# Performance work log

Hardware: AMD Instinct MI355X
Metric: run time of the kernel (lower is better)

Reference implementation:

```python
import jax, jax.numpy as jnp
import numpy as np

D = 128
EMB = 1024
B, S = 4, 4096


def setup_inputs() -> dict:
    key = jax.random.key(0)
    ks = jax.random.split(key, 7)
    scale = 1.0 / np.sqrt(EMB)
    return {
        "X": jax.random.normal(ks[0], (B, S, EMB), dtype=jnp.float32),
        "lam": jnp.float32(0.8),
        "Wq": jax.random.uniform(ks[1], (EMB, 2 * D), jnp.float32, -scale, scale),
        "bq": jax.random.uniform(ks[2], (2 * D,), jnp.float32, -scale, scale),
        "Wk": jax.random.uniform(ks[3], (EMB, 2 * D), jnp.float32, -scale, scale),
        "bk": jax.random.uniform(ks[4], (2 * D,), jnp.float32, -scale, scale),
        "Wv": jax.random.uniform(ks[5], (EMB, D), jnp.float32, -scale, scale),
        "bv": jax.random.uniform(ks[6], (D,), jnp.float32, -scale, scale),
    }


def reference(X, lam, Wq, bq, Wk, bk, Wv, bv):
    # Projections: Q,K are [B,S,2d]; V is [B,S,d]
    Q = X @ Wq + bq
    K = X @ Wk + bk
    V = X @ Wv + bv
    Q1, Q2 = Q[..., :D], Q[..., D:]
    K1, K2 = K[..., :D], K[..., D:]
    s = 1.0 / jnp.sqrt(jnp.float32(D))
    # Dual QK^T scores [B,S,S]
    A1 = jnp.einsum("bqd,bkd->bqk", Q1, K1) * s
    A2 = jnp.einsum("bqd,bkd->bqk", Q2, K2) * s
    P = jax.nn.softmax(A1, axis=-1) - lam * jax.nn.softmax(A2, axis=-1)
    return jnp.einsum("bqk,bkd->bqd", P, V)
```

## Files before the change

### kernel.cpp

```cpp
#include <hip/hip_runtime.h>
#include <hip/hip_bf16.h>


typedef __attribute__((ext_vector_type(8))) short bf16x8;
typedef __attribute__((ext_vector_type(4))) float f32x4;
typedef __attribute__((ext_vector_type(16))) float f32x16;

#define MFMA16(a, b, c) __builtin_amdgcn_mfma_f32_16x16x32_bf16((a), (b), (c), 0, 0, 0)
#define MFMA32(a, b, c) __builtin_amdgcn_mfma_f32_32x32x16_bf16((a), (b), (c), 0, 0, 0)

typedef const __attribute__((address_space(1))) void gas_void;
typedef __attribute__((address_space(3))) void las_void;
#define GLOAD16(G, L) __builtin_amdgcn_global_load_lds((gas_void*)(G), (las_void*)(L), 16, 0, 0)

__device__ __forceinline__ unsigned short f2bf(float x) {
    union { float f; unsigned u; } v; v.f = x;
    return (unsigned short)((v.u + 0x7FFFu + ((v.u >> 16) & 1u)) >> 16);
}
__device__ __forceinline__ unsigned pk2bf(float a, float b) {
    __hip_bfloat162 h = __float22bfloat162_rn(float2{a, b});
    union { __hip_bfloat162 h2; unsigned u; } cv; cv.h2 = h;
    return cv.u;
}
__device__ __forceinline__ float fexp2(float x) {
    float r; asm("v_exp_f32 %0, %1" : "=v"(r) : "v"(x)); return r;
}

__global__ __launch_bounds__(256) void wtrans_kernel(
    const float* __restrict__ Wq, const float* __restrict__ Wk,
    const float* __restrict__ Wv, unsigned short* __restrict__ Wt) {
    int tid = blockIdx.x * 256 + threadIdx.x;
    int k = tid & 1023, n = tid >> 10;
    float v;
    if (n < 256)      v = Wq[k * 256 + n];
    else if (n < 512) v = Wk[k * 256 + (n - 256)];
    else              v = Wv[k * 128 + (n - 512)];
    Wt[tid] = f2bf(v);
}

__global__ __launch_bounds__(256) void proj_kernel(
    const float* __restrict__ X, const unsigned short* __restrict__ Wt,
    const float* __restrict__ bq, const float* __restrict__ bk,
    const float* __restrict__ bv,
    unsigned short* __restrict__ Qs, unsigned short* __restrict__ Kb,
    unsigned short* __restrict__ Vb) {
    __shared__ alignas(16) char lds[16384];
    const int nt = blockIdx.y;
    const int m0 = blockIdx.x * 128;
    const int t = threadIdx.x, w = t >> 6, l = t & 63, c = l & 15, g = l >> 4;
    const int wm = w >> 1, wn = w & 1;
    const unsigned short* Wrow = Wt + (long)(nt * 128) * 1024;

    f32x4 acc[4][4];
    const f32x4 fz = {0.f, 0.f, 0.f, 0.f};
#pragma unroll
    for (int i = 0; i < 4; i++)
#pragma unroll
        for (int j = 0; j < 4; j++) acc[i][j] = fz;

    const int srow = t >> 1, sh = t & 1;
    const int sswz = (srow & 7) << 4;
    for (int k0 = 0; k0 < 1024; k0 += 32) {
        const float* xs = X + (long)(m0 + srow) * 1024 + k0 + sh * 16;
        float4 f0 = *(const float4*)(xs + 0);
        float4 f1 = *(const float4*)(xs + 4);
        float4 f2 = *(const float4*)(xs + 8);
        float4 f3 = *(const float4*)(xs + 12);
        const unsigned short* wsc = Wrow + (long)srow * 1024 + k0 + sh * 16;
        uint4 w0 = *(const uint4*)(wsc + 0);
        uint4 w1 = *(const uint4*)(wsc + 8);
        uint4 xa, xb;
        xa.x = pk2bf(f0.x, f0.y); xa.y = pk2bf(f0.z, f0.w);
        xa.z = pk2bf(f1.x, f1.y); xa.w = pk2bf(f1.z, f1.w);
        xb.x = pk2bf(f2.x, f2.y); xb.y = pk2bf(f2.z, f2.w);
        xb.z = pk2bf(f3.x, f3.y); xb.w = pk2bf(f3.z, f3.w);
        int base = srow * 64 + sh * 32;
        *(uint4*)(lds + ((base + 0) ^ sswz)) = xa;
        *(uint4*)(lds + ((base + 16) ^ sswz)) = xb;
        *(uint4*)(lds + 8192 + ((base + 0) ^ sswz)) = w0;
        *(uint4*)(lds + 8192 + ((base + 16) ^ sswz)) = w1;
        __syncthreads();

        bf16x8 af[4];
#pragma unroll
        for (int am = 0; am < 4; am++) {
            int r_ = wm * 64 + am * 16 + c;
            af[am] = *(const bf16x8*)(lds + ((r_ * 64 + g * 16) ^ ((c & 7) << 4)));
        }
#pragma unroll
        for (int bn = 0; bn < 4; bn++) {
            int r_ = wn * 64 + bn * 16 + c;
            bf16x8 bfr = *(const bf16x8*)(lds + 8192 + ((r_ * 64 + g * 16) ^ ((c & 7) << 4)));
#pragma unroll
            for (int am = 0; am < 4; am++) acc[am][bn] = MFMA16(af[am], bfr, acc[am][bn]);
        }
        __syncthreads();
    }

    const float QSCALE = 0.08838834764831845f * 1.4426950408889634f;
    const float* bias; float scale; unsigned short* outp; int ostride, ocol0, boff;
    if (nt < 2)      { bias = bq; boff = nt * 128;       scale = QSCALE; outp = Qs; ostride = 256; ocol0 = nt * 128; }
    else if (nt < 4) { bias = bk; boff = (nt - 2) * 128; scale = 1.0f;   outp = Kb; ostride = 256; ocol0 = (nt - 2) * 128; }
    else             { bias = bv; boff = 0;              scale = 1.0f;   outp = Vb; ostride = 128; ocol0 = 0; }
#pragma unroll
    for (int bn = 0; bn < 4; bn++) {
        int ncol = wn * 64 + bn * 16 + c;
        float bb = bias[boff + ncol];
#pragma unroll
        for (int am = 0; am < 4; am++) {
#pragma unroll
            for (int r = 0; r < 4; r++) {
                long row = m0 + wm * 64 + am * 16 + 4 * g + r;
                outp[row * ostride + ocol0 + ncol] = f2bf((acc[am][bn][r] + bb) * scale);
            }
        }
    }
}

__global__ __launch_bounds__(256) void vtrans_kernel(
    const unsigned short* __restrict__ Vb, unsigned short* __restrict__ Vt) {
    int tid = blockIdx.x * 256 + threadIdx.x;
    int s = tid & 4095, d = (tid >> 12) & 127, b = tid >> 19;
    Vt[tid] = Vb[(((long)b << 12) + s) * 128 + d];
}

__global__ __launch_bounds__(512) void attn3_kernel(
    const unsigned short* __restrict__ Qs, const unsigned short* __restrict__ Kb,
    const unsigned short* __restrict__ Vt,
    float* __restrict__ Po, float* __restrict__ Ps, int nsplit, int ks) {
    __shared__ alignas(16) char lds[98304];
    const int t = threadIdx.x;
    const int w = t >> 6, l = t & 63, r31 = l & 31, hi = l >> 5;
    const int wq = w >> 1, br = w & 1;

    const int total = gridDim.x;
    const int lin = (blockIdx.x & 7) * (total >> 3) + (blockIdx.x >> 3);
    const int grp = lin >> 5, qb = lin & 31;
    const int b = grp / nsplit, split = grp % nsplit;

    const long qrow = (long)b * 4096 + qb * 128 + wq * 32 + r31;
    bf16x8 qf[8];
    const unsigned short* Qp = Qs + qrow * 256 + br * 128 + hi * 8;
#pragma unroll
    for (int ds = 0; ds < 8; ds++) qf[ds] = *(const bf16x8*)(Qp + ds * 16);

    f32x16 o[4];
    const f32x16 oz = {};
#pragma unroll
    for (int dt = 0; dt < 4; dt++) o[dt] = oz;
    float m = -1e30f, s = 0.f;

    const int krow = w * 4 + (l >> 4);
    const int kc = (l & 15) * 16;
    const int ksrc_rot = (kc - krow * 16) & 255;
    const int vd = w * 16 + (l >> 2);
    const int vc = (l & 3) * 16;
    const long kbb = (long)b * 4096;
    const char* KbB = (const char*)Kb;
    const char* VtB = (const char*)Vt + ((long)b * 128 + vd) * 8192 +
                      ((vc - ((vd >> 1) & 3) * 16) & 63);
    char* dst0 = lds + w * 1024;

    const int kb0 = split * ks, kend = kb0 + ks;
#define STAGE(KB_, BUF_)                                                       \
    {                                                                          \
        const char* s1_ = KbB + (kbb + (KB_) + krow) * 512 + ksrc_rot;         \
        char* d_ = dst0 + (BUF_)*24576;                                        \
        GLOAD16(s1_, d_);                                                      \
        GLOAD16(s1_ + 256, d_ + 8192);                                         \
        GLOAD16(VtB + (long)(KB_)*2, d_ + 16384);                              \
    }

    int kro[8];
#pragma unroll
    for (int ds = 0; ds < 8; ds++)
        kro[ds] = br * 8192 + r31 * 256 + ((ds * 32 + hi * 16 + r31 * 16) & 255);
    int vro0[4], vro1[4];
#pragma unroll
    for (int dt = 0; dt < 4; dt++) {
        int vr = dt * 32 + r31, rot = ((vr >> 1) & 3) * 16;
        vro0[dt] = 16384 + vr * 64 + ((hi * 16 + rot) & 63);
        vro1[dt] = 16384 + vr * 64 + ((32 + hi * 16 + rot) & 63);
    }

    STAGE(kb0, 0);
    STAGE(kb0 + 32, 1);
    STAGE(kb0 + 64, 2);
    int cur = 0;

    for (int kb = kb0; kb < kend; kb += 32) {
        asm volatile("s_waitcnt vmcnt(6)" ::: "memory");
        __builtin_amdgcn_sched_barrier(0);
        __builtin_amdgcn_s_barrier();
        asm volatile("" ::: "memory");
        __builtin_amdgcn_sched_barrier(0);

        {
            int kn = kb + 96;
            if (kn >= kend) kn = kb0;
            STAGE(kn, (cur + 3) & 3);
        }
        const char* bufp = lds + cur * 24576;

        f32x16 pa = oz, pb_ = oz;
        __builtin_amdgcn_s_setprio(1);
#pragma unroll
        for (int ds = 0; ds < 4; ds++) {
            bf16x8 kfa = *(const bf16x8*)(bufp + kro[ds]);
            bf16x8 kfb = *(const bf16x8*)(bufp + kro[ds + 4]);
            pa = MFMA32(kfa, qf[ds], pa);
            pb_ = MFMA32(kfb, qf[ds + 4], pb_);
        }
        __builtin_amdgcn_s_setprio(0);
        f32x16 p;
#pragma unroll
        for (int i = 0; i < 16; i++) p[i] = pa[i] + pb_[i];

        float x0 = fmaxf(fmaxf(p[0], p[1]), fmaxf(p[2], p[3]));
        float x1 = fmaxf(fmaxf(p[4], p[5]), fmaxf(p[6], p[7]));
        float x2 = fmaxf(fmaxf(p[8], p[9]), fmaxf(p[10], p[11]));
        float x3 = fmaxf(fmaxf(p[12], p[13]), fmaxf(p[14], p[15]));
        float lmx = fmaxf(fmaxf(x0, x1), fmaxf(x2, x3));
        lmx = fmaxf(lmx, __shfl_xor(lmx, 32));
        if (__any(lmx > m + 8.f)) {
            float mn = fmaxf(m, lmx);
            float al = fexp2(m - mn);
            s *= al; m = mn;
#pragma unroll
            for (int dt = 0; dt < 4; dt++) o[dt] *= al;
        }
        float pe[16];
#pragma unroll
        for (int i = 0; i < 16; i++) pe[i] = fexp2(p[i] - m);
        float s0 = (pe[0] + pe[1]) + (pe[2] + pe[3]);
        float s1 = (pe[4] + pe[5]) + (pe[6] + pe[7]);
        float s2 = (pe[8] + pe[9]) + (pe[10] + pe[11]);
        float s3 = (pe[12] + pe[13]) + (pe[14] + pe[15]);
        float ps_ = (s0 + s1) + (s2 + s3);
        ps_ += __shfl_xor(ps_, 32);
        s += ps_;

        unsigned cA = pk2bf(pe[0], pe[1]), cB = pk2bf(pe[2], pe[3]);
        unsigned cC = pk2bf(pe[4], pe[5]), cD = pk2bf(pe[6], pe[7]);
        asm volatile("v_permlane32_swap_b32 %0, %1" : "+v"(cA), "+v"(cC));
        asm volatile("v_permlane32_swap_b32 %0, %1" : "+v"(cB), "+v"(cD));
        unsigned dA = pk2bf(pe[8], pe[9]), dB = pk2bf(pe[10], pe[11]);
        unsigned dC = pk2bf(pe[12], pe[13]), dD = pk2bf(pe[14], pe[15]);
        asm volatile("v_permlane32_swap_b32 %0, %1" : "+v"(dA), "+v"(dC));
        asm volatile("v_permlane32_swap_b32 %0, %1" : "+v"(dB), "+v"(dD));
        union { uint4 u; bf16x8 v; } pb0, pb1;
        pb0.u = uint4{cA, cB, cC, cD};
        pb1.u = uint4{dA, dB, dC, dD};

        __builtin_amdgcn_s_setprio(1);
#pragma unroll
        for (int dt = 0; dt < 4; dt++) {
            bf16x8 vf0 = *(const bf16x8*)(bufp + vro0[dt]);
            bf16x8 vf1 = *(const bf16x8*)(bufp + vro1[dt]);
            o[dt] = MFMA32(vf0, pb0.v, o[dt]);
            o[dt] = MFMA32(vf1, pb1.v, o[dt]);
        }
        __builtin_amdgcn_s_setprio(0);
        cur = (cur + 1) & 3;
    }

    float* po = Po + ((qrow * nsplit + split) * 2 + br) * 128;
#pragma unroll
    for (int dt = 0; dt < 4; dt++) {
#pragma unroll
        for (int rg = 0; rg < 4; rg++) {
            float4 v;
            v.x = o[dt][rg * 4 + 0];
            v.y = o[dt][rg * 4 + 1];
            v.z = o[dt][rg * 4 + 2];
            v.w = o[dt][rg * 4 + 3];
            *(float4*)(po + dt * 32 + rg * 8 + hi * 4) = v;
        }
    }
    if (hi == 0)
        *(float2*)(Ps + (qrow * nsplit + split) * 4 + br * 2) = float2{m, s};
}

__global__ __launch_bounds__(256) void combine_kernel(
    const float* __restrict__ Po, const float* __restrict__ Ps,
    const float* __restrict__ lam_p, float* __restrict__ out, int nsplit) {
    int tid = blockIdx.x * 256 + threadIdx.x;
    int q = tid >> 5, dq = (tid & 31) * 4;
    float M1 = -1e30f, M2 = -1e30f;
    for (int s = 0; s < nsplit; s++) {
        float4 st = *(const float4*)(Ps + (long)(q * nsplit + s) * 4);
        M1 = fmaxf(M1, st.x); M2 = fmaxf(M2, st.z);
    }
    float S1 = 0.f, S2 = 0.f;
    float a0 = 0.f, a1 = 0.f, a2 = 0.f, a3 = 0.f;
    float b0 = 0.f, b1 = 0.f, b2 = 0.f, b3 = 0.f;
    for (int s = 0; s < nsplit; s++) {
        float4 st = *(const float4*)(Ps + (long)(q * nsplit + s) * 4);
        float w1 = fexp2(st.x - M1), w2 = fexp2(st.z - M2);
        S1 += st.y * w1; S2 += st.w * w2;
        const float* p1 = Po + (((long)q * nsplit + s) * 2 + 0) * 128 + dq;
        const float* p2 = Po + (((long)q * nsplit + s) * 2 + 1) * 128 + dq;
        float4 v1 = *(const float4*)p1;
        float4 v2 = *(const float4*)p2;
        a0 += v1.x * w1; a1 += v1.y * w1; a2 += v1.z * w1; a3 += v1.w * w1;
        b0 += v2.x * w2; b1 += v2.y * w2; b2 += v2.z * w2; b3 += v2.w * w2;
    }
    float lam = *lam_p;
    float i1 = 1.f / S1, i2 = lam / S2;
    float4 v;
    v.x = a0 * i1 - b0 * i2;
    v.y = a1 * i1 - b1 * i2;
    v.z = a2 * i1 - b2 * i2;
    v.w = a3 * i1 - b3 * i2;
    *(float4*)(out + (long)q * 128 + dq) = v;
}

extern "C" void kernel_launch(void* const* d_in, const int* in_sizes, int n_in,
                              void* d_out, int out_size, void* d_ws, size_t ws_size,
                              hipStream_t stream) {
    const float* X   = (const float*)d_in[0];
    const float* lam = (const float*)d_in[1];
    const float* Wq  = (const float*)d_in[2];
    const float* bq  = (const float*)d_in[3];
    const float* Wk  = (const float*)d_in[4];
    const float* bk  = (const float*)d_in[5];
    const float* Wv  = (const float*)d_in[6];
    const float* bv  = (const float*)d_in[7];
    char* ws = (char*)d_ws;
    unsigned short* Qs = (unsigned short*)(ws);
    unsigned short* Kb = (unsigned short*)(ws + (8u << 20));
    unsigned short* Vb = (unsigned short*)(ws + (16u << 20));
    unsigned short* Vt = (unsigned short*)(ws + (20u << 20));
    unsigned short* Wt = (unsigned short*)(ws + (24u << 20));
    const size_t base = (size_t)26 << 20;
    const size_t NQ = 16384;
    int nsplit = 1;
    if (ws_size >= base + NQ * 4 * 2 * 128 * 4 + NQ * 4 * 4 * 4)      nsplit = 4;
    else if (ws_size >= base + NQ * 2 * 2 * 128 * 4 + NQ * 2 * 4 * 4) nsplit = 2;
    float* Po = (float*)(ws + base);
    float* Ps = (float*)(ws + base + NQ * (size_t)nsplit * 2 * 128 * 4);

    wtrans_kernel<<<2560, 256, 0, stream>>>(Wq, Wk, Wv, Wt);
    proj_kernel<<<dim3(128, 5), 256, 0, stream>>>(X, Wt, bq, bk, bv, Qs, Kb, Vb);
    vtrans_kernel<<<8192, 256, 0, stream>>>(Vb, Vt);
    attn3_kernel<<<128 * nsplit, 512, 0, stream>>>(Qs, Kb, Vt, Po, Ps,
                                                   nsplit, 4096 / nsplit);
    combine_kernel<<<2048, 256, 0, stream>>>(Po, Ps, lam, (float*)d_out, nsplit);
}
```

Before: 174.9 us.

## Software-pipeline QK^T of next tile with softmax and PV of current tile

Restructures the attention main loop so the QK^T MFMAs for tile i+1 are issued alongside the softmax and PV MFMAs for tile i, using two ping-pong score registers and a loop unrolled by two. The aim is to overlap MFMA work with exp/reduction VALU work and hide LDS latency. Barrier waits change from vmcnt(6) to vmcnt(3), and the s_setprio hints are dropped. It raises register pressure with an extra f32x16 live score tile and assumes the tile count is even and at least 2.

```diff
diff --git a/kernel.cpp b/kernel.cpp
--- a/kernel.cpp
+++ b/kernel.cpp
@@ -162,6 +162,7 @@
     char* dst0 = lds + w * 1024;
 
     const int kb0 = split * ks, kend = kb0 + ks;
+    const int nt = ks >> 5;
 #define STAGE(KB_, BUF_)                                                       \
     {                                                                          \
         const char* s1_ = KbB + (kbb + (KB_) + krow) * 512 + ksrc_rot;         \
@@ -183,86 +184,98 @@
         vro1[dt] = 16384 + vr * 64 + ((32 + hi * 16 + rot) & 63);
     }
 
+#define FENCE_TOP(N)                                                           \
+    asm volatile("s_waitcnt vmcnt(" #N ")" ::: "memory");                      \
+    __builtin_amdgcn_sched_barrier(0);                                         \
+    __builtin_amdgcn_s_barrier();                                              \
+    __builtin_amdgcn_sched_barrier(0);
+
+#define QKTILE(PN, TI)                                                         \
+    {                                                                          \
+        const char* kp_ = lds + ((TI) & 3) * 24576;                            \
+        f32x16 qa_ = oz, qb_ = oz;                                             \
+        _Pragma("unroll") for (int d_ = 0; d_ < 4; d_++) {                     \
+            bf16x8 ka_ = *(const bf16x8*)(kp_ + kro[d_]);                      \
+            bf16x8 kb_ = *(const bf16x8*)(kp_ + kro[d_ + 4]);                  \
+            qa_ = MFMA32(ka_, qf[d_], qa_);                                    \
+            qb_ = MFMA32(kb_, qf[d_ + 4], qb_);                                \
+        }                                                                      \
+        _Pragma("unroll") for (int i_ = 0; i_ < 16; i_++)                      \
+            PN[i_] = qa_[i_] + qb_[i_];                                        \
+    }
+
+#define SOFTPV(PC, TI)                                                         \
+    {                                                                          \
+        float x0 = fmaxf(fmaxf(PC[0], PC[1]), fmaxf(PC[2], PC[3]));            \
+        float x1 = fmaxf(fmaxf(PC[4], PC[5]), fmaxf(PC[6], PC[7]));            \
+        float x2 = fmaxf(fmaxf(PC[8], PC[9]), fmaxf(PC[10], PC[11]));          \
+        float x3 = fmaxf(fmaxf(PC[12], PC[13]), fmaxf(PC[14], PC[15]));        \
+        float lmx = fmaxf(fmaxf(x0, x1), fmaxf(x2, x3));                       \
+        lmx = fmaxf(lmx, __shfl_xor(lmx, 32));                                 \
+        if (__any(lmx > m + 8.f)) {                                            \
+            float mn = fmaxf(m, lmx);                                          \
+            float al = fexp2(m - mn);                                          \
+            s *= al; m = mn;                                                   \
+            _Pragma("unroll") for (int dt_ = 0; dt_ < 4; dt_++) o[dt_] *= al;  \
+        }                                                                      \
+        float pe[16];                                                          \
+        _Pragma("unroll") for (int i_ = 0; i_ < 16; i_++)                      \
+            pe[i_] = fexp2(PC[i_] - m);                                        \
+        float s0 = (pe[0] + pe[1]) + (pe[2] + pe[3]);                          \
+        float s1 = (pe[4] + pe[5]) + (pe[6] + pe[7]);                          \
+        float s2 = (pe[8] + pe[9]) + (pe[10] + pe[11]);                        \
+        float s3 = (pe[12] + pe[13]) + (pe[14] + pe[15]);                      \
+        float ps_ = (s0 + s1) + (s2 + s3);                                     \
+        ps_ += __shfl_xor(ps_, 32);                                            \
+        s += ps_;                                                              \
+        unsigned cA = pk2bf(pe[0], pe[1]), cB = pk2bf(pe[2], pe[3]);           \
+        unsigned cC = pk2bf(pe[4], pe[5]), cD = pk2bf(pe[6], pe[7]);           \
+        asm volatile("v_permlane32_swap_b32 %0, %1" : "+v"(cA), "+v"(cC));     \
+        asm volatile("v_permlane32_swap_b32 %0, %1" : "+v"(cB), "+v"(cD));     \
+        unsigned dA = pk2bf(pe[8], pe[9]), dB = pk2bf(pe[10], pe[11]);         \
+        unsigned dC = pk2bf(pe[12], pe[13]), dD = pk2bf(pe[14], pe[15]);       \
+        asm volatile("v_permlane32_swap_b32 %0, %1" : "+v"(dA), "+v"(dC));     \
+        asm volatile("v_permlane32_swap_b32 %0, %1" : "+v"(dB), "+v"(dD));     \
+        union { uint4 u; bf16x8 v; } pb0_, pb1_;                               \
+        pb0_.u = uint4{cA, cB, cC, cD};                                        \
+        pb1_.u = uint4{dA, dB, dC, dD};                                        \
+        const char* vb_ = lds + ((TI) & 3) * 24576;                            \
+        _Pragma("unroll") for (int dt_ = 0; dt_ < 4; dt_++) {                  \
+            bf16x8 vf0 = *(const bf16x8*)(vb_ + vro0[dt_]);                    \
+            bf16x8 vf1 = *(const bf16x8*)(vb_ + vro1[dt_]);                    \
+            o[dt_] = MFMA32(vf0, pb0_.v, o[dt_]);                              \
+            o[dt_] = MFMA32(vf1, pb1_.v, o[dt_]);                              \
+        }                                                                      \
+    }
+
+#define STEP(PC, PN, I)                                                        \
+    {                                                                          \
+        FENCE_TOP(3)                                                           \
+        {                                                                      \
+            int i3_ = (I) + 3;                                                 \
+            int kn_ = (i3_ < nt) ? kb0 + (i3_ << 5) : kb0;                     \
+            STAGE(kn_, i3_ & 3);                                               \
+        }                                                                      \
+        QKTILE(PN, (I) + 1)                                                    \
+        SOFTPV(PC, (I))                                                        \
+    }
+
     STAGE(kb0, 0);
     STAGE(kb0 + 32, 1);
     STAGE(kb0 + 64, 2);
-    int cur = 0;
-
-    for (int kb = kb0; kb < kend; kb += 32) {
-        asm volatile("s_waitcnt vmcnt(6)" ::: "memory");
-        __builtin_amdgcn_sched_barrier(0);
-        __builtin_amdgcn_s_barrier();
-        asm volatile("" ::: "memory");
-        __builtin_amdgcn_sched_barrier(0);
-
-        {
-            int kn = kb + 96;
-            if (kn >= kend) kn = kb0;
-            STAGE(kn, (cur + 3) & 3);
-        }
-        const char* bufp = lds + cur * 24576;
-
-        f32x16 pa = oz, pb_ = oz;
-        __builtin_amdgcn_s_setprio(1);
-#pragma unroll
-        for (int ds = 0; ds < 4; ds++) {
-            bf16x8 kfa = *(const bf16x8*)(bufp + kro[ds]);
-            bf16x8 kfb = *(const bf16x8*)(bufp + kro[ds + 4]);
-            pa = MFMA32(kfa, qf[ds], pa);
-            pb_ = MFMA32(kfb, qf[ds + 4], pb_);
-        }
-        __builtin_amdgcn_s_setprio(0);
-        f32x16 p;
-#pragma unroll
-        for (int i = 0; i < 16; i++) p[i] = pa[i] + pb_[i];
-
-        float x0 = fmaxf(fmaxf(p[0], p[1]), fmaxf(p[2], p[3]));
-        float x1 = fmaxf(fmaxf(p[4], p[5]), fmaxf(p[6], p[7]));
-        float x2 = fmaxf(fmaxf(p[8], p[9]), fmaxf(p[10], p[11]));
-        float x3 = fmaxf(fmaxf(p[12], p[13]), fmaxf(p[14], p[15]));
-        float lmx = fmaxf(fmaxf(x0, x1), fmaxf(x2, x3));
-        lmx = fmaxf(lmx, __shfl_xor(lmx, 32));
-        if (__any(lmx > m + 8.f)) {
-            float mn = fmaxf(m, lmx);
-            float al = fexp2(m - mn);
-            s *= al; m = mn;
-#pragma unroll
-            for (int dt = 0; dt < 4; dt++) o[dt] *= al;
-        }
-        float pe[16];
-#pragma unroll
-        for (int i = 0; i < 16; i++) pe[i] = fexp2(p[i] - m);
-        float s0 = (pe[0] + pe[1]) + (pe[2] + pe[3]);
-        float s1 = (pe[4] + pe[5]) + (pe[6] + pe[7]);
-        float s2 = (pe[8] + pe[9]) + (pe[10] + pe[11]);
-        float s3 = (pe[12] + pe[13]) + (pe[14] + pe[15]);
-        float ps_ = (s0 + s1) + (s2 + s3);
-        ps_ += __shfl_xor(ps_, 32);
-        s += ps_;
-
-        unsigned cA = pk2bf(pe[0], pe[1]), cB = pk2bf(pe[2], pe[3]);
-        unsigned cC = pk2bf(pe[4], pe[5]), cD = pk2bf(pe[6], pe[7]);
-        asm volatile("v_permlane32_swap_b32 %0, %1" : "+v"(cA), "+v"(cC));
-        asm volatile("v_permlane32_swap_b32 %0, %1" : "+v"(cB), "+v"(cD));
-        unsigned dA = pk2bf(pe[8], pe[9]), dB = pk2bf(pe[10], pe[11]);
-        unsigned dC = pk2bf(pe[12], pe[13]), dD = pk2bf(pe[14], pe[15]);
-        asm volatile("v_permlane32_swap_b32 %0, %1" : "+v"(dA), "+v"(dC));
-        asm volatile("v_permlane32_swap_b32 %0, %1" : "+v"(dB), "+v"(dD));
-        union { uint4 u; bf16x8 v; } pb0, pb1;
-        pb0.u = uint4{cA, cB, cC, cD};
-        pb1.u = uint4{dA, dB, dC, dD};
-
-        __builtin_amdgcn_s_setprio(1);
-#pragma unroll
-        for (int dt = 0; dt < 4; dt++) {
-            bf16x8 vf0 = *(const bf16x8*)(bufp + vro0[dt]);
-            bf16x8 vf1 = *(const bf16x8*)(bufp + vro1[dt]);
-            o[dt] = MFMA32(vf0, pb0.v, o[dt]);
-            o[dt] = MFMA32(vf1, pb1.v, o[dt]);
-        }
-        __builtin_amdgcn_s_setprio(0);
-        cur = (cur + 1) & 3;
-    }
+    f32x16 pA, pB;
+    FENCE_TOP(6)
+    QKTILE(pA, 0)
+
+    int it = 0;
+    for (; it + 2 < nt; it += 2) {
+        STEP(pA, pB, it)
+        STEP(pB, pA, it + 1)
+    }
+    STEP(pA, pB, nt - 2)
+    FENCE_TOP(3)
+    SOFTPV(pB, nt - 1)
+    asm volatile("s_waitcnt vmcnt(0)" ::: "memory");
 
     float* po = Po + ((qrow * nsplit + split) * 2 + br) * 128;
 #pragma unroll
@@ -279,6 +292,11 @@
     }
     if (hi == 0)
         *(float2*)(Ps + (qrow * nsplit + split) * 4 + br * 2) = float2{m, s};
+#undef STAGE
+#undef FENCE_TOP
+#undef QKTILE
+#undef SOFTPV
+#undef STEP
 }
 
 __global__ __launch_bounds__(256) void combine_kernel(
```

After: 171.0 us. 2.3% less time.

## Split attention blocks per softmax branch with triple-buffered K/V staging

Applied to the files above, without the earlier changes.

The attention kernel now runs 256-thread blocks that each handle a single softmax branch for 128 query rows, where before one 512-thread block handled both branches. Each block stages only its half of K, so LDS per buffer shrinks and the pipeline drops from four buffers to three. Twice as many blocks are launched, which is meant to raise occupancy and balance the load across CUs. In exchange, every V tile is now loaded by both branch blocks, which doubles V traffic, and prefetch depth is reduced by one stage.

```diff
diff --git a/kernel.cpp b/kernel.cpp
--- a/kernel.cpp
+++ b/kernel.cpp
@@ -124,21 +124,23 @@
     Vt[tid] = Vb[(((long)b << 12) + s) * 128 + d];
 }
 
-__global__ __launch_bounds__(512) void attn3_kernel(
+__global__ __launch_bounds__(256) void attn3_kernel(
     const unsigned short* __restrict__ Qs, const unsigned short* __restrict__ Kb,
     const unsigned short* __restrict__ Vt,
     float* __restrict__ Po, float* __restrict__ Ps, int nsplit, int ks) {
-    __shared__ alignas(16) char lds[98304];
+    __shared__ alignas(16) char lds[49152];
     const int t = threadIdx.x;
     const int w = t >> 6, l = t & 63, r31 = l & 31, hi = l >> 5;
-    const int wq = w >> 1, br = w & 1;
 
     const int total = gridDim.x;
     const int lin = (blockIdx.x & 7) * (total >> 3) + (blockIdx.x >> 3);
-    const int grp = lin >> 5, qb = lin & 31;
-    const int b = grp / nsplit, split = grp % nsplit;
-
-    const long qrow = (long)b * 4096 + qb * 128 + wq * 32 + r31;
+    const int qb = lin & 31;
+    const int g2 = lin >> 5;
+    const int br = g2 & 1;
+    const int sp = g2 >> 1;
+    const int split = sp % nsplit, b = sp / nsplit;
+
+    const long qrow = (long)b * 4096 + qb * 128 + w * 32 + r31;
     bf16x8 qf[8];
     const unsigned short* Qp = Qs + qrow * 256 + br * 128 + hi * 8;
 #pragma unroll
@@ -150,57 +152,55 @@
     for (int dt = 0; dt < 4; dt++) o[dt] = oz;
     float m = -1e30f, s = 0.f;
 
-    const int krow = w * 4 + (l >> 4);
-    const int kc = (l & 15) * 16;
-    const int ksrc_rot = (kc - krow * 16) & 255;
-    const int vd = w * 16 + (l >> 2);
-    const int vc = (l & 3) * 16;
+    const int krowA = t >> 4;
+    const int kcolS = (((t & 15) * 16) - krowA * 16) & 255;
+    const int vdA = t >> 2;
+    const int vcolS = (((t & 3) * 16) - (((vdA >> 1) & 3) * 16)) & 63;
     const long kbb = (long)b * 4096;
-    const char* KbB = (const char*)Kb;
-    const char* VtB = (const char*)Vt + ((long)b * 128 + vd) * 8192 +
-                      ((vc - ((vd >> 1) & 3) * 16) & 63);
+    const char* kSrc0 = (const char*)Kb + (kbb + krowA) * 512 + br * 256 + kcolS;
+    const char* vSrc0 = (const char*)Vt + ((long)b * 128 + vdA) * 8192 + vcolS;
     char* dst0 = lds + w * 1024;
 
-    const int kb0 = split * ks, kend = kb0 + ks;
+    const int kb0 = split * ks;
+    const int nt = ks >> 5;
 #define STAGE(KB_, BUF_)                                                       \
     {                                                                          \
-        const char* s1_ = KbB + (kbb + (KB_) + krow) * 512 + ksrc_rot;         \
-        char* d_ = dst0 + (BUF_)*24576;                                        \
-        GLOAD16(s1_, d_);                                                      \
-        GLOAD16(s1_ + 256, d_ + 8192);                                         \
-        GLOAD16(VtB + (long)(KB_)*2, d_ + 16384);                              \
+        const char* kp_ = kSrc0 + (long)(KB_)*512;                             \
+        const char* vp_ = vSrc0 + (long)(KB_)*2;                               \
+        char* d_ = dst0 + (BUF_)*16384;                                        \
+        GLOAD16(kp_, d_);                                                      \
+        GLOAD16(kp_ + 8192, d_ + 4096);                                        \
+        GLOAD16(vp_, d_ + 8192);                                               \
+        GLOAD16(vp_ + 524288, d_ + 12288);                                     \
     }
 
     int kro[8];
 #pragma unroll
     for (int ds = 0; ds < 8; ds++)
-        kro[ds] = br * 8192 + r31 * 256 + ((ds * 32 + hi * 16 + r31 * 16) & 255);
+        kro[ds] = r31 * 256 + ((ds * 32 + hi * 16 + r31 * 16) & 255);
     int vro0[4], vro1[4];
 #pragma unroll
     for (int dt = 0; dt < 4; dt++) {
         int vr = dt * 32 + r31, rot = ((vr >> 1) & 3) * 16;
-        vro0[dt] = 16384 + vr * 64 + ((hi * 16 + rot) & 63);
-        vro1[dt] = 16384 + vr * 64 + ((32 + hi * 16 + rot) & 63);
+        vro0[dt] = 8192 + vr * 64 + ((hi * 16 + rot) & 63);
+        vro1[dt] = 8192 + vr * 64 + ((32 + hi * 16 + rot) & 63);
     }
 
     STAGE(kb0, 0);
     STAGE(kb0 + 32, 1);
-    STAGE(kb0 + 64, 2);
-    int cur = 0;
-
-    for (int kb = kb0; kb < kend; kb += 32) {
-        asm volatile("s_waitcnt vmcnt(6)" ::: "memory");
+    int cb = 0, sb = 2;
+
+    for (int it = 0; it < nt; it++) {
+        asm volatile("s_waitcnt vmcnt(4)" ::: "memory");
         __builtin_amdgcn_sched_barrier(0);
         __builtin_amdgcn_s_barrier();
-        asm volatile("" ::: "memory");
         __builtin_amdgcn_sched_barrier(0);
-
         {
-            int kn = kb + 96;
-            if (kn >= kend) kn = kb0;
-            STAGE(kn, (cur + 3) & 3);
-        }
-        const char* bufp = lds + cur * 24576;
+            int i2 = it + 2;
+            int kn = (i2 < nt) ? kb0 + (i2 << 5) : kb0;
+            STAGE(kn, sb);
+        }
+        const char* bufp = lds + cb * 16384;
 
         f32x16 pa = oz, pb_ = oz;
         __builtin_amdgcn_s_setprio(1);
@@ -216,11 +216,13 @@
 #pragma unroll
         for (int i = 0; i < 16; i++) p[i] = pa[i] + pb_[i];
 
-        float x0 = fmaxf(fmaxf(p[0], p[1]), fmaxf(p[2], p[3]));
-        float x1 = fmaxf(fmaxf(p[4], p[5]), fmaxf(p[6], p[7]));
-        float x2 = fmaxf(fmaxf(p[8], p[9]), fmaxf(p[10], p[11]));
-        float x3 = fmaxf(fmaxf(p[12], p[13]), fmaxf(p[14], p[15]));
-        float lmx = fmaxf(fmaxf(x0, x1), fmaxf(x2, x3));
+        float m0_ = fmaxf(fmaxf(p[0], p[1]), p[2]);
+        float m1_ = fmaxf(fmaxf(p[3], p[4]), p[5]);
+        float m2_ = fmaxf(fmaxf(p[6], p[7]), p[8]);
+        float m3_ = fmaxf(fmaxf(p[9], p[10]), p[11]);
+        float m4_ = fmaxf(fmaxf(p[12], p[13]), p[14]);
+        float lmx = fmaxf(fmaxf(fmaxf(fmaxf(m0_, m1_), m2_),
+                                fmaxf(m3_, m4_)), p[15]);
         lmx = fmaxf(lmx, __shfl_xor(lmx, 32));
         if (__any(lmx > m + 8.f)) {
             float mn = fmaxf(m, lmx);
@@ -261,8 +263,10 @@
             o[dt] = MFMA32(vf1, pb1.v, o[dt]);
         }
         __builtin_amdgcn_s_setprio(0);
-        cur = (cur + 1) & 3;
-    }
+        cb = (cb == 2) ? 0 : cb + 1;
+        sb = (sb == 2) ? 0 : sb + 1;
+    }
+    asm volatile("s_waitcnt vmcnt(0)" ::: "memory");
 
     float* po = Po + ((qrow * nsplit + split) * 2 + br) * 128;
 #pragma unroll
@@ -279,6 +283,7 @@
     }
     if (hi == 0)
         *(float2*)(Ps + (qrow * nsplit + split) * 4 + br * 2) = float2{m, s};
+#undef STAGE
 }
 
 __global__ __launch_bounds__(256) void combine_kernel(
@@ -343,7 +348,7 @@
     wtrans_kernel<<<2560, 256, 0, stream>>>(Wq, Wk, Wv, Wt);
     proj_kernel<<<dim3(128, 5), 256, 0, stream>>>(X, Wt, bq, bk, bv, Qs, Kb, Vb);
     vtrans_kernel<<<8192, 256, 0, stream>>>(Vb, Vt);
-    attn3_kernel<<<128 * nsplit, 512, 0, stream>>>(Qs, Kb, Vt, Po, Ps,
+    attn3_kernel<<<256 * nsplit, 256, 0, stream>>>(Qs, Kb, Vt, Po, Ps,
                                                    nsplit, 4096 / nsplit);
     combine_kernel<<<2048, 256, 0, stream>>>(Po, Ps, lam, (float*)d_out, nsplit);
 }
```

After: 170.8 us. -2.4%, faster.

## Pre-convert X to bf16 and use async LDS-staged MFMA32 projection; tile V transpose

Applied to the files above, without the earlier changes.

Adds a kernel that converts X to bf16 once, plus a new projection GEMM that streams bf16 X and weight tiles into LDS with global_load_lds double buffering and 32x32 MFMAs. The old projection read fp32 X directly. The V transpose is rewritten to go through an LDS tile with 16-byte vector loads and stores, replacing the per-element gather. In exchange there is an extra launch and an extra round-trip of X through memory, and the bf16 X buffer reuses the Po workspace region.

```diff
diff --git a/kernel.cpp b/kernel.cpp
--- a/kernel.cpp
+++ b/kernel.cpp
@@ -36,6 +36,110 @@
     else if (n < 512) v = Wk[k * 256 + (n - 256)];
     else              v = Wv[k * 128 + (n - 512)];
     Wt[tid] = f2bf(v);
+}
+
+__global__ __launch_bounds__(256) void xcvt_kernel(
+    const float* __restrict__ X, unsigned short* __restrict__ Xb) {
+    long i = ((long)blockIdx.x * 256 + threadIdx.x) * 8;
+    float4 a = *(const float4*)(X + i);
+    float4 b = *(const float4*)(X + i + 4);
+    uint4 u;
+    u.x = pk2bf(a.x, a.y); u.y = pk2bf(a.z, a.w);
+    u.z = pk2bf(b.x, b.y); u.w = pk2bf(b.z, b.w);
+    *(uint4*)(Xb + i) = u;
+}
+
+__global__ __launch_bounds__(256) void proj2_kernel(
+    const unsigned short* __restrict__ Xb, const unsigned short* __restrict__ Wt,
+    const float* __restrict__ bq, const float* __restrict__ bk,
+    const float* __restrict__ bv,
+    unsigned short* __restrict__ Qs, unsigned short* __restrict__ Kb,
+    unsigned short* __restrict__ Vb) {
+    __shared__ alignas(16) char lds[65536];
+    const int nt = blockIdx.y;
+    const int m0 = blockIdx.x * 128;
+    const int t = threadIdx.x, w = t >> 6, l = t & 63, r31 = l & 31, hi = l >> 5;
+    const int wm = w >> 1, wn = w & 1;
+
+    const int rowA = t >> 3;
+    const int acolS = (((t & 7) * 16) - (rowA & 7) * 16) & 127;
+    const char* aSrc0 = (const char*)Xb + (long)(m0 + rowA) * 2048 + acolS;
+    const char* bSrc0 = (const char*)Wt + (long)(nt * 128 + rowA) * 2048 + acolS;
+    char* dst0 = lds + w * 1024;
+
+#define PSTAGE(ST_, BUF_)                                                      \
+    {                                                                          \
+        const char* a_ = aSrc0 + (long)(ST_)*128;                              \
+        const char* b_ = bSrc0 + (long)(ST_)*128;                              \
+        char* d_ = dst0 + (BUF_)*32768;                                        \
+        GLOAD16(a_, d_);                                                       \
+        GLOAD16(a_ + 65536, d_ + 4096);                                        \
+        GLOAD16(a_ + 131072, d_ + 8192);                                       \
+        GLOAD16(a_ + 196608, d_ + 12288);                                      \
+        GLOAD16(b_, d_ + 16384);                                               \
+        GLOAD16(b_ + 65536, d_ + 20480);                                       \
+        GLOAD16(b_ + 131072, d_ + 24576);                                      \
+        GLOAD16(b_ + 196608, d_ + 28672);                                      \
+    }
+
+    int aro[2][4], bro[2][4];
+#pragma unroll
+    for (int mi = 0; mi < 2; mi++)
+#pragma unroll
+        for (int ks = 0; ks < 4; ks++) {
+            int rot = (ks * 32 + hi * 16 + (r31 & 7) * 16) & 127;
+            aro[mi][ks] = (wm * 64 + mi * 32 + r31) * 128 + rot;
+            bro[mi][ks] = 16384 + (wn * 64 + mi * 32 + r31) * 128 + rot;
+        }
+
+    f32x16 acc[2][2];
+    const f32x16 oz = {};
+    acc[0][0] = oz; acc[0][1] = oz; acc[1][0] = oz; acc[1][1] = oz;
+
+    PSTAGE(0, 0);
+    for (int st = 0; st < 16; st++) {
+        asm volatile("s_waitcnt vmcnt(0)" ::: "memory");
+        __builtin_amdgcn_sched_barrier(0);
+        __builtin_amdgcn_s_barrier();
+        __builtin_amdgcn_sched_barrier(0);
+        if (st + 1 < 16) PSTAGE(st + 1, (st + 1) & 1);
+        const char* bp = lds + (st & 1) * 32768;
+        __builtin_amdgcn_s_setprio(1);
+#pragma unroll
+        for (int ks = 0; ks < 4; ks++) {
+            bf16x8 a0 = *(const bf16x8*)(bp + aro[0][ks]);
+            bf16x8 a1 = *(const bf16x8*)(bp + aro[1][ks]);
+            bf16x8 b0 = *(const bf16x8*)(bp + bro[0][ks]);
+            bf16x8 b1 = *(const bf16x8*)(bp + bro[1][ks]);
+            acc[0][0] = MFMA32(a0, b0, acc[0][0]);
+            acc[0][1] = MFMA32(a0, b1, acc[0][1]);
+            acc[1][0] = MFMA32(a1, b0, acc[1][0]);
+            acc[1][1] = MFMA32(a1, b1, acc[1][1]);
+        }
+        __builtin_amdgcn_s_setprio(0);
+    }
+#undef PSTAGE
+
+    const float QSCALE = 0.08838834764831845f * 1.4426950408889634f;
+    const float* bias; float scale; unsigned short* outp; int ostride, ocol0, boff;
+    if (nt < 2)      { bias = bq; boff = nt * 128;       scale = QSCALE; outp = Qs; ostride = 256; ocol0 = nt * 128; }
+    else if (nt < 4) { bias = bk; boff = (nt - 2) * 128; scale = 1.0f;   outp = Kb; ostride = 256; ocol0 = (nt - 2) * 128; }
+    else             { bias = bv; boff = 0;              scale = 1.0f;   outp = Vb; ostride = 128; ocol0 = 0; }
+#pragma unroll
+    for (int ni = 0; ni < 2; ni++) {
+        int ncol = wn * 64 + ni * 32 + r31;
+        float bb = bias[boff + ncol];
+#pragma unroll
+        for (int mi = 0; mi < 2; mi++) {
+#pragma unroll
+            for (int reg = 0; reg < 16; reg++) {
+                int mrow = wm * 64 + mi * 32 + (reg & 3) + 8 * (reg >> 2) + 4 * hi;
+                long row = m0 + mrow;
+                outp[row * ostride + ocol0 + ncol] =
+                    f2bf((acc[mi][ni][reg] + bb) * scale);
+            }
+        }
+    }
 }
 
 __global__ __launch_bounds__(256) void proj_kernel(
@@ -119,9 +223,28 @@
 
 __global__ __launch_bounds__(256) void vtrans_kernel(
     const unsigned short* __restrict__ Vb, unsigned short* __restrict__ Vt) {
-    int tid = blockIdx.x * 256 + threadIdx.x;
-    int s = tid & 4095, d = (tid >> 12) & 127, b = tid >> 19;
-    Vt[tid] = Vb[(((long)b << 12) + s) * 128 + d];
+    __shared__ unsigned short lds[64][72];
+    const int bid = blockIdx.x;
+    const int db = bid & 1, sb = (bid >> 1) & 63, b = bid >> 7;
+    const int s0 = sb * 64, d0 = db * 64;
+    const int t = threadIdx.x;
+    const int r = t >> 2, c4 = t & 3;
+    const unsigned short* src = Vb + ((long)(b * 4096 + s0 + r)) * 128 + d0;
+    uint4 u0 = *(const uint4*)(src + c4 * 8);
+    uint4 u1 = *(const uint4*)(src + (c4 + 4) * 8);
+    *(uint4*)(&lds[r][c4 * 8]) = u0;
+    *(uint4*)(&lds[r][(c4 + 4) * 8]) = u1;
+    __syncthreads();
+    const int dd = t >> 2;
+    unsigned short* dst = Vt + ((long)(b * 128 + d0 + dd)) * 4096 + s0;
+#pragma unroll
+    for (int cc2 = 0; cc2 < 2; cc2++) {
+        int cc = c4 + cc2 * 4;
+        unsigned short tmp[8];
+#pragma unroll
+        for (int j = 0; j < 8; j++) tmp[j] = lds[cc * 8 + j][dd];
+        *(uint4*)(dst + cc * 8) = *(const uint4*)tmp;
+    }
 }
 
 __global__ __launch_bounds__(512) void attn3_kernel(
@@ -194,7 +317,6 @@
         __builtin_amdgcn_s_barrier();
         asm volatile("" ::: "memory");
         __builtin_amdgcn_sched_barrier(0);
-
         {
             int kn = kb + 96;
             if (kn >= kend) kn = kb0;
@@ -279,6 +401,7 @@
     }
     if (hi == 0)
         *(float2*)(Ps + (qrow * nsplit + split) * 4 + br * 2) = float2{m, s};
+#undef STAGE
 }
 
 __global__ __launch_bounds__(256) void combine_kernel(
@@ -339,10 +462,18 @@
     else if (ws_size >= base + NQ * 2 * 2 * 128 * 4 + NQ * 2 * 4 * 4) nsplit = 2;
     float* Po = (float*)(ws + base);
     float* Ps = (float*)(ws + base + NQ * (size_t)nsplit * 2 * 128 * 4);
+    unsigned short* Xb = (unsigned short*)(ws + base);
 
     wtrans_kernel<<<2560, 256, 0, stream>>>(Wq, Wk, Wv, Wt);
-    proj_kernel<<<dim3(128, 5), 256, 0, stream>>>(X, Wt, bq, bk, bv, Qs, Kb, Vb);
-    vtrans_kernel<<<8192, 256, 0, stream>>>(Vb, Vt);
+    if (nsplit >= 2) {
+        xcvt_kernel<<<8192, 256, 0, stream>>>(X, Xb);
+        proj2_kernel<<<dim3(128, 5), 256, 0, stream>>>(Xb, Wt, bq, bk, bv,
+                                                       Qs, Kb, Vb);
+    } else {
+        proj_kernel<<<dim3(128, 5), 256, 0, stream>>>(X, Wt, bq, bk, bv,
+                                                      Qs, Kb, Vb);
+    }
+    vtrans_kernel<<<512, 256, 0, stream>>>(Vb, Vt);
     attn3_kernel<<<128 * nsplit, 512, 0, stream>>>(Qs, Kb, Vt, Po, Ps,
                                                    nsplit, 4096 / nsplit);
     combine_kernel<<<2048, 256, 0, stream>>>(Po, Ps, lam, (float*)d_out, nsplit);
```

Measured after the change: 172.7 us. About the same (-1.3%).
